# Performance work log

Measured on AMD Instinct MI355X. Metric: run time of the kernel, lower is better.

## Reference

```python
import jax, jax.numpy as jnp
import numpy as np

B, L, D, H = 2, 2048, 1024, 16
HD = D // H  # head dim = 64


def setup_inputs() -> dict:
    key = jax.random.key(0)
    ks = jax.random.split(key, 6)
    s = 0.02
    return {
        "hidden_states": jax.random.normal(ks[0], (B, L, D), jnp.float32),
        "attention_mask": jnp.zeros((B, 1, 1, L), jnp.float32),
        "Wq": jax.random.normal(ks[1], (D, D), jnp.float32) * s,
        "bq": jnp.zeros((D,), jnp.float32),
        "Wk": jax.random.normal(ks[2], (D, D), jnp.float32) * s,
        "bk": jnp.zeros((D,), jnp.float32),
        "Wv": jax.random.normal(ks[3], (D, D), jnp.float32) * s,
        "bv": jnp.zeros((D,), jnp.float32),
        "Wo": jax.random.normal(ks[4], (D, D), jnp.float32) * s,
        "bo": jnp.zeros((D,), jnp.float32),
    }


def reference(hidden_states, attention_mask, Wq, bq, Wk, bk, Wv, bv, Wo, bo):
    # Linear projections (torch Linear: x @ W.T + b; here W stored as [in,out])
    q = hidden_states @ Wq + bq  # [B,L,D]
    k = hidden_states @ Wk + bk
    v = hidden_states @ Wv + bv

    def split_heads(x):  # [B,L,D] -> [B,H,L,HD]
        return x.reshape(B, L, H, HD).transpose(0, 2, 1, 3)

    q, k, v = split_heads(q), split_heads(k), split_heads(v)

    scores = jnp.einsum("bhqd,bhkd->bhqk", q, k) / jnp.sqrt(
        jnp.asarray(HD, q.dtype)
    )
    scores = scores + attention_mask  # additive mask, broadcast [B,1,1,L]
    pdtype = scores.dtype
    # fp32 upcast around softmax, as in the original module
    probs = jax.nn.softmax(scores.astype(jnp.float32), axis=-1).astype(pdtype)
    # dropout prob = 0 (eval) -> identity; head_mask=None
    ctx = jnp.einsum("bhqk,bhkd->bhqd", probs, v)  # [B,H,L,HD]
    ctx = ctx.transpose(0, 2, 1, 3).reshape(B, L, D)
    out = ctx @ Wo + bo  # BertSelfOutput_preLN dense (dropout=0)
    return out
```

## Files before the change

### kernel.cpp

```cpp
#include <hip/hip_runtime.h>

#define BB 2
#define LL 2048
#define DDIM 1024
#define HH 16
#define HDIM 64
#define MM (BB*LL)
#define KK 1024
#define LOG2E 1.44269504f

typedef __attribute__((ext_vector_type(8))) short s8v;
typedef __attribute__((ext_vector_type(8))) unsigned short u8v;
typedef __attribute__((ext_vector_type(4))) float f4v;

__device__ __forceinline__ unsigned short f2bf(float f) {
    unsigned int u = __float_as_uint(f);
    u += 0x7fffu + ((u >> 16) & 1u);
    return (unsigned short)(u >> 16);
}

__device__ __forceinline__ float fexp2(float x) { return __builtin_amdgcn_exp2f(x); }

__device__ __forceinline__ void gld_lds16(const unsigned short* g, unsigned short* l) {
    __builtin_amdgcn_global_load_lds(
        (const __attribute__((address_space(1))) unsigned int*)g,
        (__attribute__((address_space(3))) unsigned int*)l, 16, 0, 0);
}

__global__ __launch_bounds__(256) void prep(
        const float* __restrict__ X,
        const float* __restrict__ Wq, const float* __restrict__ Wk,
        const float* __restrict__ Wv, const float* __restrict__ Wo,
        unsigned short* __restrict__ Xb,
        unsigned short* __restrict__ WqT, unsigned short* __restrict__ WkT,
        unsigned short* __restrict__ WvT, unsigned short* __restrict__ WoT) {
    __shared__ float lds[64][65];
    const int blk = blockIdx.x, t = threadIdx.x;
    if (blk < 4096) {
        int i = blk * 256 + t;
        float4 v = ((const float4*)X)[i];
        ushort4 r;
        r.x = f2bf(v.x); r.y = f2bf(v.y); r.z = f2bf(v.z); r.w = f2bf(v.w);
        ((ushort4*)Xb)[i] = r;
        return;
    }
    const int tb = blk - 4096;
    const int w = tb >> 8;
    const int tile = tb & 255;
    const int k0 = (tile >> 4) * 64, n0 = (tile & 15) * 64;
    const float* src; unsigned short* dst;
    switch (w) {
        case 0: src = Wq; dst = WqT; break;
        case 1: src = Wk; dst = WkT; break;
        case 2: src = Wv; dst = WvT; break;
        default: src = Wo; dst = WoT; break;
    }
    #pragma unroll
    for (int j = 0; j < 4; ++j) {
        int r = (t >> 4) + 16*j, c = (t & 15) * 4;
        float4 v = *(const float4*)(src + (size_t)(k0 + r) * DDIM + n0 + c);
        lds[r][c] = v.x; lds[r][c+1] = v.y; lds[r][c+2] = v.z; lds[r][c+3] = v.w;
    }
    __syncthreads();
    #pragma unroll
    for (int j = 0; j < 2; ++j) {
        int rr = (t >> 3) + 32*j, cc = (t & 7) * 8;
        u8v o;
        #pragma unroll
        for (int i = 0; i < 8; ++i) o[i] = f2bf(lds[cc + i][rr]);
        *(u8v*)(dst + (size_t)(n0 + rr) * KK + k0 + cc) = o;
    }
}

__device__ __forceinline__ void gemm_core(const unsigned short* __restrict__ A,
                                          const unsigned short* __restrict__ BT,
                                          int Mbase, int Nbase,
                                          unsigned short* As, unsigned short* Bs,
                                          f4v acc[4][4]) {
    const int t = threadIdx.x;
    const int lane = t & 63, wave = t >> 6;
    const int wm = wave & 1, wn = wave >> 1;
    const int l15 = lane & 15, quad = lane >> 4;
    const int srow = t >> 2, schunk = (t & 3) * 8;

    #pragma unroll
    for (int mt = 0; mt < 4; ++mt)
        #pragma unroll
        for (int nt = 0; nt < 4; ++nt)
            acc[mt][nt] = f4v{0.f, 0.f, 0.f, 0.f};

    const unsigned short* gA0 = A  + (size_t)(Mbase + srow)      * KK + schunk;
    const unsigned short* gA1 = A  + (size_t)(Mbase + 64 + srow) * KK + schunk;
    const unsigned short* gB0 = BT + (size_t)(Nbase + srow)      * KK + schunk;
    const unsigned short* gB1 = BT + (size_t)(Nbase + 64 + srow) * KK + schunk;
    unsigned short* lA0 = As + t*8;
    unsigned short* lA1 = As + 64*32 + t*8;
    unsigned short* lB0 = Bs + t*8;
    unsigned short* lB1 = Bs + 64*32 + t*8;

    for (int kb = 0; kb < KK; kb += 32) {
        __syncthreads();
        gld_lds16(gA0 + kb, lA0);
        gld_lds16(gA1 + kb, lA1);
        gld_lds16(gB0 + kb, lB0);
        gld_lds16(gB1 + kb, lB1);
        __syncthreads();
        s8v af[4], bfv[4];
        #pragma unroll
        for (int mt = 0; mt < 4; ++mt)
            af[mt] = *(const s8v*)(As + (wm*64 + mt*16 + l15)*32 + quad*8);
        #pragma unroll
        for (int nt = 0; nt < 4; ++nt)
            bfv[nt] = *(const s8v*)(Bs + (wn*64 + nt*16 + l15)*32 + quad*8);
        #pragma unroll
        for (int mt = 0; mt < 4; ++mt)
            #pragma unroll
            for (int nt = 0; nt < 4; ++nt)
                acc[mt][nt] = __builtin_amdgcn_mfma_f32_16x16x32_bf16(af[mt], bfv[nt], acc[mt][nt], 0, 0, 0);
    }
}

__global__ __launch_bounds__(256) void qkv_gemm(
        const unsigned short* __restrict__ Xb,
        const unsigned short* __restrict__ WqT, const unsigned short* __restrict__ WkT,
        const unsigned short* __restrict__ WvT,
        const float* __restrict__ bq, const float* __restrict__ bk, const float* __restrict__ bv,
        unsigned short* __restrict__ Qh, unsigned short* __restrict__ Kh,
        unsigned short* __restrict__ Vt) {
    __shared__ alignas(16) unsigned short As[128*32];
    __shared__ alignas(16) unsigned short Bs[128*32];
    const int mode = blockIdx.z;
    const unsigned short* BT = (mode == 0) ? WqT : (mode == 1) ? WkT : WvT;
    const float* bias        = (mode == 0) ? bq  : (mode == 1) ? bk  : bv;
    unsigned short* out      = (mode == 0) ? Qh  : (mode == 1) ? Kh  : Vt;
    const int Mbase = blockIdx.y * 128, Nbase = blockIdx.x * 128;

    f4v acc[4][4];
    gemm_core(Xb, BT, Mbase, Nbase, As, Bs, acc);

    const int lane = threadIdx.x & 63, wave = threadIdx.x >> 6;
    const int wm = wave & 1, wn = wave >> 1, l15 = lane & 15, quad = lane >> 4;
    #pragma unroll
    for (int mt = 0; mt < 4; ++mt)
        #pragma unroll
        for (int nt = 0; nt < 4; ++nt)
            #pragma unroll
            for (int r = 0; r < 4; ++r) {
                int gm = Mbase + wm*64 + mt*16 + quad*4 + r;
                int gn = Nbase + wn*64 + nt*16 + l15;
                float v = acc[mt][nt][r] + bias[gn];
                int bb = gm >> 11, ll = gm & 2047;
                int hh = gn >> 6,  dd = gn & 63;
                if (mode == 2)
                    out[((size_t)(bb*HH + hh)*HDIM + dd)*LL + ll] = f2bf(v);
                else
                    out[((size_t)(bb*HH + hh)*LL + ll)*HDIM + dd] = f2bf(v);
            }
}

__global__ __launch_bounds__(256) void attn(
        const unsigned short* __restrict__ Qh, const unsigned short* __restrict__ Kh,
        const unsigned short* __restrict__ Vt, const float* __restrict__ mask,
        unsigned short* __restrict__ ctx) {
    __shared__ alignas(16) unsigned short Ks[64*72];
    __shared__ alignas(16) unsigned short Vs[64*72];
    __shared__ alignas(16) unsigned short P [4*16*72];

    const int t = threadIdx.x, lane = t & 63, wave = t >> 6;
    const int l15 = lane & 15, quad = lane >> 4;

    const int n = blockIdx.x;
    const int bh = (n & 7) * 4 + ((n >> 3) & 3);
    const int qblk = n >> 5;
    const int b = bh >> 4, h = bh & 15;

    const unsigned short* Qb = Qh + (size_t)bh * LL * HDIM;
    const unsigned short* Kb = Kh + (size_t)bh * LL * HDIM;
    const unsigned short* Vb = Vt + (size_t)bh * HDIM * LL;
    const float* mb = mask + (size_t)b * LL;
    const int q0 = qblk * 64 + wave * 16;
    unsigned short* Pw = P + wave * 16 * 72;

    const int srow = t >> 2, scol = (t & 3) * 16;

    s8v qf[2];
    #pragma unroll
    for (int hf = 0; hf < 2; ++hf)
        qf[hf] = *(const s8v*)(Qb + (size_t)(q0 + l15)*HDIM + hf*32 + quad*8);

    f4v o[4];
    #pragma unroll
    for (int dt = 0; dt < 4; ++dt) o[dt] = f4v{0.f, 0.f, 0.f, 0.f};
    float rs[4];
    #pragma unroll
    for (int r = 0; r < 4; ++r) rs[r] = 0.f;

    const float C1 = 0.125f * LOG2E;

    for (int kt = 0; kt < LL; kt += 64) {
        float4 ka = *(const float4*)(Kb + (size_t)(kt + srow)*HDIM + scol);
        float4 kb2 = *(const float4*)(Kb + (size_t)(kt + srow)*HDIM + scol + 8);
        float4 va = *(const float4*)(Vb + (size_t)srow*LL + kt + scol);
        float4 vb2 = *(const float4*)(Vb + (size_t)srow*LL + kt + scol + 8);
        float mv[4];
        #pragma unroll
        for (int nt = 0; nt < 4; ++nt)
            mv[nt] = mb[kt + nt*16 + l15] * LOG2E;

        __syncthreads();
        *(float4*)(Ks + srow*72 + scol)     = ka;
        *(float4*)(Ks + srow*72 + scol + 8) = kb2;
        *(float4*)(Vs + srow*72 + scol)     = va;
        *(float4*)(Vs + srow*72 + scol + 8) = vb2;
        __syncthreads();

        f4v sac[4];
        #pragma unroll
        for (int nt = 0; nt < 4; ++nt) {
            sac[nt] = f4v{0.f, 0.f, 0.f, 0.f};
            #pragma unroll
            for (int hf = 0; hf < 2; ++hf) {
                s8v kf = *(const s8v*)(Ks + (nt*16 + l15)*72 + hf*32 + quad*8);
                sac[nt] = __builtin_amdgcn_mfma_f32_16x16x32_bf16(qf[hf], kf, sac[nt], 0, 0, 0);
            }
        }
        #pragma unroll
        for (int nt = 0; nt < 4; ++nt)
            #pragma unroll
            for (int r = 0; r < 4; ++r) {
                float p = fexp2(sac[nt][r] * C1 + mv[nt]);
                rs[r] += p;
                Pw[(quad*4 + r)*72 + nt*16 + l15] = f2bf(p);
            }
        s8v pf[2];
        #pragma unroll
        for (int hf = 0; hf < 2; ++hf)
            pf[hf] = *(const s8v*)(Pw + l15*72 + hf*32 + quad*8);
        #pragma unroll
        for (int dt = 0; dt < 4; ++dt)
            #pragma unroll
            for (int hf = 0; hf < 2; ++hf) {
                s8v vfr = *(const s8v*)(Vs + (dt*16 + l15)*72 + hf*32 + quad*8);
                o[dt] = __builtin_amdgcn_mfma_f32_16x16x32_bf16(pf[hf], vfr, o[dt], 0, 0, 0);
            }
    }

    #pragma unroll
    for (int r = 0; r < 4; ++r) {
        float s0 = rs[r];
        s0 += __shfl_xor(s0, 1);
        s0 += __shfl_xor(s0, 2);
        s0 += __shfl_xor(s0, 4);
        s0 += __shfl_xor(s0, 8);
        float inv = 1.0f / s0;
        int q = q0 + quad*4 + r;
        size_t base = ((size_t)b*LL + q)*DDIM + h*HDIM;
        #pragma unroll
        for (int dt = 0; dt < 4; ++dt)
            ctx[base + dt*16 + l15] = f2bf(o[dt][r] * inv);
    }
}

__global__ __launch_bounds__(256) void out_gemm(
        const unsigned short* __restrict__ Cb, const unsigned short* __restrict__ WoT,
        const float* __restrict__ bo, float* __restrict__ out) {
    __shared__ alignas(16) unsigned short As[128*32];
    __shared__ alignas(16) unsigned short Bs[64*32];
    const int t = threadIdx.x;
    const int lane = t & 63, wave = t >> 6;
    const int wm = wave & 1, wn = wave >> 1;
    const int l15 = lane & 15, quad = lane >> 4;
    const int srow = t >> 2, schunk = (t & 3) * 8;
    const int Mbase = blockIdx.y * 128, Nbase = blockIdx.x * 64;

    f4v acc[4][2];
    #pragma unroll
    for (int mt = 0; mt < 4; ++mt)
        #pragma unroll
        for (int nt = 0; nt < 2; ++nt)
            acc[mt][nt] = f4v{0.f, 0.f, 0.f, 0.f};

    const unsigned short* gA0 = Cb  + (size_t)(Mbase + srow)      * KK + schunk;
    const unsigned short* gA1 = Cb  + (size_t)(Mbase + 64 + srow) * KK + schunk;
    const unsigned short* gB0 = WoT + (size_t)(Nbase + srow)      * KK + schunk;
    unsigned short* lA0 = As + t*8;
    unsigned short* lA1 = As + 64*32 + t*8;
    unsigned short* lB0 = Bs + t*8;

    for (int kb = 0; kb < KK; kb += 32) {
        __syncthreads();
        gld_lds16(gA0 + kb, lA0);
        gld_lds16(gA1 + kb, lA1);
        gld_lds16(gB0 + kb, lB0);
        __syncthreads();
        s8v af[4], bfv[2];
        #pragma unroll
        for (int mt = 0; mt < 4; ++mt)
            af[mt] = *(const s8v*)(As + (wm*64 + mt*16 + l15)*32 + quad*8);
        #pragma unroll
        for (int nt = 0; nt < 2; ++nt)
            bfv[nt] = *(const s8v*)(Bs + (wn*32 + nt*16 + l15)*32 + quad*8);
        #pragma unroll
        for (int mt = 0; mt < 4; ++mt)
            #pragma unroll
            for (int nt = 0; nt < 2; ++nt)
                acc[mt][nt] = __builtin_amdgcn_mfma_f32_16x16x32_bf16(af[mt], bfv[nt], acc[mt][nt], 0, 0, 0);
    }

    #pragma unroll
    for (int mt = 0; mt < 4; ++mt)
        #pragma unroll
        for (int nt = 0; nt < 2; ++nt)
            #pragma unroll
            for (int r = 0; r < 4; ++r) {
                int gm = Mbase + wm*64 + mt*16 + quad*4 + r;
                int gn = Nbase + wn*32 + nt*16 + l15;
                out[(size_t)gm*DDIM + gn] = acc[mt][nt][r] + bo[gn];
            }
}

extern "C" void kernel_launch(void* const* d_in, const int* in_sizes, int n_in,
                              void* d_out, int out_size, void* d_ws, size_t ws_size,
                              hipStream_t stream) {
    const float* X    = (const float*)d_in[0];
    const float* mask = (const float*)d_in[1];
    const float* Wq   = (const float*)d_in[2];
    const float* bq   = (const float*)d_in[3];
    const float* Wk   = (const float*)d_in[4];
    const float* bk   = (const float*)d_in[5];
    const float* Wv   = (const float*)d_in[6];
    const float* bv   = (const float*)d_in[7];
    const float* Wo   = (const float*)d_in[8];
    const float* bo   = (const float*)d_in[9];
    float* out = (float*)d_out;

    char* ws = (char*)d_ws;
    unsigned short* Xb  = (unsigned short*)(ws);
    unsigned short* WqT = (unsigned short*)(ws + (8u  << 20));
    unsigned short* WkT = (unsigned short*)(ws + (10u << 20));
    unsigned short* WvT = (unsigned short*)(ws + (12u << 20));
    unsigned short* WoT = (unsigned short*)(ws + (14u << 20));
    unsigned short* Qh  = (unsigned short*)(ws + (16u << 20));
    unsigned short* Kh  = (unsigned short*)(ws + (24u << 20));
    unsigned short* Vt  = (unsigned short*)(ws + (32u << 20));
    unsigned short* Cb  = Xb;

    prep     <<<dim3(5120),    dim3(256), 0, stream>>>(X, Wq, Wk, Wv, Wo, Xb, WqT, WkT, WvT, WoT);
    qkv_gemm <<<dim3(8,32,3),  dim3(256), 0, stream>>>(Xb, WqT, WkT, WvT, bq, bk, bv, Qh, Kh, Vt);
    attn     <<<dim3(1024),    dim3(256), 0, stream>>>(Qh, Kh, Vt, mask, Cb);
    out_gemm <<<dim3(16,32),   dim3(256), 0, stream>>>(Cb, WoT, bo, out);
}
```

Measured before the change: 220.3 us.

## Use 32x32 MFMA with 128-query attention tiles and K=64 GEMM stages

The attention kernel now gives each wave 32 queries instead of 16 and switches to 32x32x16 bf16 MFMA. That halves the block count and doubles reuse of each K/V tile staged in LDS. Both GEMMs now stage 64-wide K slices per iteration, which halves the number of barrier pairs. In exchange the attention kernel needs more registers and a larger P buffer, which may lower occupancy, and the GEMMs use twice the LDS.

```diff
diff --git a/kernel.cpp b/kernel.cpp
--- a/kernel.cpp
+++ b/kernel.cpp
@@ -12,6 +12,7 @@
 typedef __attribute__((ext_vector_type(8))) short s8v;
 typedef __attribute__((ext_vector_type(8))) unsigned short u8v;
 typedef __attribute__((ext_vector_type(4))) float f4v;
+typedef __attribute__((ext_vector_type(16))) float f16v;
 
 __device__ __forceinline__ unsigned short f2bf(float f) {
     unsigned int u = __float_as_uint(f);
@@ -93,30 +94,35 @@
     const unsigned short* gA1 = A  + (size_t)(Mbase + 64 + srow) * KK + schunk;
     const unsigned short* gB0 = BT + (size_t)(Nbase + srow)      * KK + schunk;
     const unsigned short* gB1 = BT + (size_t)(Nbase + 64 + srow) * KK + schunk;
-    unsigned short* lA0 = As + t*8;
-    unsigned short* lA1 = As + 64*32 + t*8;
-    unsigned short* lB0 = Bs + t*8;
-    unsigned short* lB1 = Bs + 64*32 + t*8;
-
-    for (int kb = 0; kb < KK; kb += 32) {
-        __syncthreads();
-        gld_lds16(gA0 + kb, lA0);
-        gld_lds16(gA1 + kb, lA1);
-        gld_lds16(gB0 + kb, lB0);
-        gld_lds16(gB1 + kb, lB1);
-        __syncthreads();
-        s8v af[4], bfv[4];
-        #pragma unroll
-        for (int mt = 0; mt < 4; ++mt)
-            af[mt] = *(const s8v*)(As + (wm*64 + mt*16 + l15)*32 + quad*8);
-        #pragma unroll
-        for (int nt = 0; nt < 4; ++nt)
-            bfv[nt] = *(const s8v*)(Bs + (wn*64 + nt*16 + l15)*32 + quad*8);
-        #pragma unroll
-        for (int mt = 0; mt < 4; ++mt)
+
+    for (int kb = 0; kb < KK; kb += 64) {
+        __syncthreads();
+        gld_lds16(gA0 + kb,      As + t*8);
+        gld_lds16(gA1 + kb,      As + 2048 + t*8);
+        gld_lds16(gA0 + kb + 32, As + 4096 + t*8);
+        gld_lds16(gA1 + kb + 32, As + 4096 + 2048 + t*8);
+        gld_lds16(gB0 + kb,      Bs + t*8);
+        gld_lds16(gB1 + kb,      Bs + 2048 + t*8);
+        gld_lds16(gB0 + kb + 32, Bs + 4096 + t*8);
+        gld_lds16(gB1 + kb + 32, Bs + 4096 + 2048 + t*8);
+        __syncthreads();
+        #pragma unroll
+        for (int kk = 0; kk < 2; ++kk) {
+            const unsigned short* Ab = As + kk*4096;
+            const unsigned short* Bb = Bs + kk*4096;
+            s8v af[4], bfv[4];
+            #pragma unroll
+            for (int mt = 0; mt < 4; ++mt)
+                af[mt] = *(const s8v*)(Ab + (wm*64 + mt*16 + l15)*32 + quad*8);
             #pragma unroll
             for (int nt = 0; nt < 4; ++nt)
-                acc[mt][nt] = __builtin_amdgcn_mfma_f32_16x16x32_bf16(af[mt], bfv[nt], acc[mt][nt], 0, 0, 0);
+                bfv[nt] = *(const s8v*)(Bb + (wn*64 + nt*16 + l15)*32 + quad*8);
+            #pragma unroll
+            for (int mt = 0; mt < 4; ++mt)
+                #pragma unroll
+                for (int nt = 0; nt < 4; ++nt)
+                    acc[mt][nt] = __builtin_amdgcn_mfma_f32_16x16x32_bf16(af[mt], bfv[nt], acc[mt][nt], 0, 0, 0);
+        }
     }
 }
 
@@ -127,8 +133,8 @@
         const float* __restrict__ bq, const float* __restrict__ bk, const float* __restrict__ bv,
         unsigned short* __restrict__ Qh, unsigned short* __restrict__ Kh,
         unsigned short* __restrict__ Vt) {
-    __shared__ alignas(16) unsigned short As[128*32];
-    __shared__ alignas(16) unsigned short Bs[128*32];
+    __shared__ alignas(16) unsigned short As[128*64];
+    __shared__ alignas(16) unsigned short Bs[128*64];
     const int mode = blockIdx.z;
     const unsigned short* BT = (mode == 0) ? WqT : (mode == 1) ? WkT : WvT;
     const float* bias        = (mode == 0) ? bq  : (mode == 1) ? bk  : bv;
@@ -164,48 +170,48 @@
         unsigned short* __restrict__ ctx) {
     __shared__ alignas(16) unsigned short Ks[64*72];
     __shared__ alignas(16) unsigned short Vs[64*72];
-    __shared__ alignas(16) unsigned short P [4*16*72];
+    __shared__ alignas(16) unsigned short P [4*32*72];
 
     const int t = threadIdx.x, lane = t & 63, wave = t >> 6;
-    const int l15 = lane & 15, quad = lane >> 4;
+    const int l31 = lane & 31, hgrp = lane >> 5;
 
     const int n = blockIdx.x;
     const int bh = (n & 7) * 4 + ((n >> 3) & 3);
     const int qblk = n >> 5;
-    const int b = bh >> 4, h = bh & 15;
+    const int b = bh >> 4, hh = bh & 15;
 
     const unsigned short* Qb = Qh + (size_t)bh * LL * HDIM;
     const unsigned short* Kb = Kh + (size_t)bh * LL * HDIM;
     const unsigned short* Vb = Vt + (size_t)bh * HDIM * LL;
     const float* mb = mask + (size_t)b * LL;
-    const int q0 = qblk * 64 + wave * 16;
-    unsigned short* Pw = P + wave * 16 * 72;
+    const int q0 = qblk * 128 + wave * 32;
+    unsigned short* Pw = P + wave * 32 * 72;
 
     const int srow = t >> 2, scol = (t & 3) * 16;
 
-    s8v qf[2];
-    #pragma unroll
-    for (int hf = 0; hf < 2; ++hf)
-        qf[hf] = *(const s8v*)(Qb + (size_t)(q0 + l15)*HDIM + hf*32 + quad*8);
-
-    f4v o[4];
-    #pragma unroll
-    for (int dt = 0; dt < 4; ++dt) o[dt] = f4v{0.f, 0.f, 0.f, 0.f};
-    float rs[4];
-    #pragma unroll
-    for (int r = 0; r < 4; ++r) rs[r] = 0.f;
+    s8v qf[4];
+    #pragma unroll
+    for (int hf = 0; hf < 4; ++hf)
+        qf[hf] = *(const s8v*)(Qb + (size_t)(q0 + l31)*HDIM + hf*16 + hgrp*8);
+
+    f16v o[2];
+    #pragma unroll
+    for (int nc = 0; nc < 2; ++nc)
+        #pragma unroll
+        for (int r = 0; r < 16; ++r) o[nc][r] = 0.f;
+    float rs[16];
+    #pragma unroll
+    for (int r = 0; r < 16; ++r) rs[r] = 0.f;
 
     const float C1 = 0.125f * LOG2E;
 
     for (int kt = 0; kt < LL; kt += 64) {
-        float4 ka = *(const float4*)(Kb + (size_t)(kt + srow)*HDIM + scol);
+        float4 ka  = *(const float4*)(Kb + (size_t)(kt + srow)*HDIM + scol);
         float4 kb2 = *(const float4*)(Kb + (size_t)(kt + srow)*HDIM + scol + 8);
-        float4 va = *(const float4*)(Vb + (size_t)srow*LL + kt + scol);
+        float4 va  = *(const float4*)(Vb + (size_t)srow*LL + kt + scol);
         float4 vb2 = *(const float4*)(Vb + (size_t)srow*LL + kt + scol + 8);
-        float mv[4];
-        #pragma unroll
-        for (int nt = 0; nt < 4; ++nt)
-            mv[nt] = mb[kt + nt*16 + l15] * LOG2E;
+        float mv0 = mb[kt + l31] * LOG2E;
+        float mv1 = mb[kt + 32 + l31] * LOG2E;
 
         __syncthreads();
         *(float4*)(Ks + srow*72 + scol)     = ka;
@@ -214,58 +220,65 @@
         *(float4*)(Vs + srow*72 + scol + 8) = vb2;
         __syncthreads();
 
-        f4v sac[4];
-        #pragma unroll
-        for (int nt = 0; nt < 4; ++nt) {
-            sac[nt] = f4v{0.f, 0.f, 0.f, 0.f};
-            #pragma unroll
-            for (int hf = 0; hf < 2; ++hf) {
-                s8v kf = *(const s8v*)(Ks + (nt*16 + l15)*72 + hf*32 + quad*8);
-                sac[nt] = __builtin_amdgcn_mfma_f32_16x16x32_bf16(qf[hf], kf, sac[nt], 0, 0, 0);
-            }
-        }
-        #pragma unroll
-        for (int nt = 0; nt < 4; ++nt)
-            #pragma unroll
-            for (int r = 0; r < 4; ++r) {
-                float p = fexp2(sac[nt][r] * C1 + mv[nt]);
+        f16v sac[2];
+        #pragma unroll
+        for (int kc = 0; kc < 2; ++kc) {
+            #pragma unroll
+            for (int r = 0; r < 16; ++r) sac[kc][r] = 0.f;
+            #pragma unroll
+            for (int hf = 0; hf < 4; ++hf) {
+                s8v kf = *(const s8v*)(Ks + (kc*32 + l31)*72 + hf*16 + hgrp*8);
+                sac[kc] = __builtin_amdgcn_mfma_f32_32x32x16_bf16(qf[hf], kf, sac[kc], 0, 0, 0);
+            }
+        }
+        #pragma unroll
+        for (int kc = 0; kc < 2; ++kc) {
+            float mvv = kc ? mv1 : mv0;
+            #pragma unroll
+            for (int r = 0; r < 16; ++r) {
+                float p = fexp2(sac[kc][r] * C1 + mvv);
                 rs[r] += p;
-                Pw[(quad*4 + r)*72 + nt*16 + l15] = f2bf(p);
-            }
-        s8v pf[2];
-        #pragma unroll
-        for (int hf = 0; hf < 2; ++hf)
-            pf[hf] = *(const s8v*)(Pw + l15*72 + hf*32 + quad*8);
-        #pragma unroll
-        for (int dt = 0; dt < 4; ++dt)
-            #pragma unroll
-            for (int hf = 0; hf < 2; ++hf) {
-                s8v vfr = *(const s8v*)(Vs + (dt*16 + l15)*72 + hf*32 + quad*8);
-                o[dt] = __builtin_amdgcn_mfma_f32_16x16x32_bf16(pf[hf], vfr, o[dt], 0, 0, 0);
-            }
-    }
-
-    #pragma unroll
-    for (int r = 0; r < 4; ++r) {
+                int row = (r & 3) + 8*(r >> 2) + 4*hgrp;
+                Pw[row*72 + kc*32 + l31] = f2bf(p);
+            }
+        }
+        #pragma unroll
+        for (int kt16 = 0; kt16 < 4; ++kt16) {
+            s8v pf = *(const s8v*)(Pw + l31*72 + kt16*16 + hgrp*8);
+            #pragma unroll
+            for (int nc = 0; nc < 2; ++nc) {
+                s8v vf = *(const s8v*)(Vs + (nc*32 + l31)*72 + kt16*16 + hgrp*8);
+                o[nc] = __builtin_amdgcn_mfma_f32_32x32x16_bf16(pf, vf, o[nc], 0, 0, 0);
+            }
+        }
+    }
+
+    #pragma unroll
+    for (int r = 0; r < 16; ++r) {
         float s0 = rs[r];
         s0 += __shfl_xor(s0, 1);
         s0 += __shfl_xor(s0, 2);
         s0 += __shfl_xor(s0, 4);
         s0 += __shfl_xor(s0, 8);
-        float inv = 1.0f / s0;
-        int q = q0 + quad*4 + r;
-        size_t base = ((size_t)b*LL + q)*DDIM + h*HDIM;
-        #pragma unroll
-        for (int dt = 0; dt < 4; ++dt)
-            ctx[base + dt*16 + l15] = f2bf(o[dt][r] * inv);
+        s0 += __shfl_xor(s0, 16);
+        rs[r] = 1.0f / s0;
+    }
+    #pragma unroll
+    for (int r = 0; r < 16; ++r) {
+        int row = (r & 3) + 8*(r >> 2) + 4*hgrp;
+        int q = q0 + row;
+        size_t base = ((size_t)b*LL + q)*DDIM + hh*HDIM;
+        #pragma unroll
+        for (int nc = 0; nc < 2; ++nc)
+            ctx[base + nc*32 + l31] = f2bf(o[nc][r] * rs[r]);
     }
 }
 
 __global__ __launch_bounds__(256) void out_gemm(
         const unsigned short* __restrict__ Cb, const unsigned short* __restrict__ WoT,
         const float* __restrict__ bo, float* __restrict__ out) {
-    __shared__ alignas(16) unsigned short As[128*32];
-    __shared__ alignas(16) unsigned short Bs[64*32];
+    __shared__ alignas(16) unsigned short As[128*64];
+    __shared__ alignas(16) unsigned short Bs[64*64];
     const int t = threadIdx.x;
     const int lane = t & 63, wave = t >> 6;
     const int wm = wave & 1, wn = wave >> 1;
@@ -283,28 +296,33 @@
     const unsigned short* gA0 = Cb  + (size_t)(Mbase + srow)      * KK + schunk;
     const unsigned short* gA1 = Cb  + (size_t)(Mbase + 64 + srow) * KK + schunk;
     const unsigned short* gB0 = WoT + (size_t)(Nbase + srow)      * KK + schunk;
-    unsigned short* lA0 = As + t*8;
-    unsigned short* lA1 = As + 64*32 + t*8;
-    unsigned short* lB0 = Bs + t*8;
-
-    for (int kb = 0; kb < KK; kb += 32) {
-        __syncthreads();
-        gld_lds16(gA0 + kb, lA0);
-        gld_lds16(gA1 + kb, lA1);
-        gld_lds16(gB0 + kb, lB0);
-        __syncthreads();
-        s8v af[4], bfv[2];
-        #pragma unroll
-        for (int mt = 0; mt < 4; ++mt)
-            af[mt] = *(const s8v*)(As + (wm*64 + mt*16 + l15)*32 + quad*8);
-        #pragma unroll
-        for (int nt = 0; nt < 2; ++nt)
-            bfv[nt] = *(const s8v*)(Bs + (wn*32 + nt*16 + l15)*32 + quad*8);
-        #pragma unroll
-        for (int mt = 0; mt < 4; ++mt)
+
+    for (int kb = 0; kb < KK; kb += 64) {
+        __syncthreads();
+        gld_lds16(gA0 + kb,      As + t*8);
+        gld_lds16(gA1 + kb,      As + 2048 + t*8);
+        gld_lds16(gA0 + kb + 32, As + 4096 + t*8);
+        gld_lds16(gA1 + kb + 32, As + 4096 + 2048 + t*8);
+        gld_lds16(gB0 + kb,      Bs + t*8);
+        gld_lds16(gB0 + kb + 32, Bs + 2048 + t*8);
+        __syncthreads();
+        #pragma unroll
+        for (int kk = 0; kk < 2; ++kk) {
+            const unsigned short* Ab = As + kk*4096;
+            const unsigned short* Bb = Bs + kk*2048;
+            s8v af[4], bfv[2];
+            #pragma unroll
+            for (int mt = 0; mt < 4; ++mt)
+                af[mt] = *(const s8v*)(Ab + (wm*64 + mt*16 + l15)*32 + quad*8);
             #pragma unroll
             for (int nt = 0; nt < 2; ++nt)
-                acc[mt][nt] = __builtin_amdgcn_mfma_f32_16x16x32_bf16(af[mt], bfv[nt], acc[mt][nt], 0, 0, 0);
+                bfv[nt] = *(const s8v*)(Bb + (wn*32 + nt*16 + l15)*32 + quad*8);
+            #pragma unroll
+            for (int mt = 0; mt < 4; ++mt)
+                #pragma unroll
+                for (int nt = 0; nt < 2; ++nt)
+                    acc[mt][nt] = __builtin_amdgcn_mfma_f32_16x16x32_bf16(af[mt], bfv[nt], acc[mt][nt], 0, 0, 0);
+        }
     }
 
     #pragma unroll
@@ -347,6 +365,6 @@
 
     prep     <<<dim3(5120),    dim3(256), 0, stream>>>(X, Wq, Wk, Wv, Wo, Xb, WqT, WkT, WvT, WoT);
     qkv_gemm <<<dim3(8,32,3),  dim3(256), 0, stream>>>(Xb, WqT, WkT, WvT, bq, bk, bv, Qh, Kh, Vt);
-    attn     <<<dim3(1024),    dim3(256), 0, stream>>>(Qh, Kh, Vt, mask, Cb);
+    attn     <<<dim3(512),     dim3(256), 0, stream>>>(Qh, Kh, Vt, mask, Cb);
     out_gemm <<<dim3(16,32),   dim3(256), 0, stream>>>(Cb, WoT, bo, out);
 }
```

After: 226.0 us. 2.6% more time.
